# Kernel tuning notes

Hardware: AMD Instinct MI355X
Metric: run time of the kernel (lower is better)

## Reference

```python
import jax, jax.numpy as jnp
import numpy as np
from jax import lax

INPUT_SIZE = 256
HIDDEN = 256
NUM_CLASSES = 100
BLANK_ID = 3
B, T = 512, 128
STEPS = 26  # batch_max_length + 1


def setup_inputs() -> dict:
    key = jax.random.key(0)
    ks = jax.random.split(key, 16)
    s = lambda fan_in: 1.0 / np.sqrt(fan_in)
    inp = {
        "batch_H": jax.random.normal(ks[0], (B, T, INPUT_SIZE), dtype=jnp.float32),
        "text": jax.random.randint(ks[1], (B, STEPS), 0, NUM_CLASSES),
        "batch_max_length": 25,
        # AttentionCell params
        "W_i2h": jax.random.uniform(ks[2], (HIDDEN, INPUT_SIZE), minval=-s(INPUT_SIZE), maxval=s(INPUT_SIZE)),
        "W_h2h": jax.random.uniform(ks[3], (HIDDEN, HIDDEN), minval=-s(HIDDEN), maxval=s(HIDDEN)),
        "b_h2h": jax.random.uniform(ks[4], (HIDDEN,), minval=-s(HIDDEN), maxval=s(HIDDEN)),
        "W_score": jax.random.uniform(ks[5], (1, HIDDEN), minval=-s(HIDDEN), maxval=s(HIDDEN)),
        # LSTMCell params (PyTorch layout: gates order i, f, g, o)
        "W_ih": jax.random.uniform(ks[6], (4 * HIDDEN, INPUT_SIZE + NUM_CLASSES), minval=-s(HIDDEN), maxval=s(HIDDEN)),
        "W_hh": jax.random.uniform(ks[7], (4 * HIDDEN, HIDDEN), minval=-s(HIDDEN), maxval=s(HIDDEN)),
        "b_ih": jax.random.uniform(ks[8], (4 * HIDDEN,), minval=-s(HIDDEN), maxval=s(HIDDEN)),
        "b_hh": jax.random.uniform(ks[9], (4 * HIDDEN,), minval=-s(HIDDEN), maxval=s(HIDDEN)),
        # generator
        "W_gen": jax.random.uniform(ks[10], (NUM_CLASSES, HIDDEN), minval=-s(HIDDEN), maxval=s(HIDDEN)),
        "b_gen": jax.random.uniform(ks[11], (NUM_CLASSES,), minval=-s(HIDDEN), maxval=s(HIDDEN)),
    }
    return inp


def reference(batch_H, text, batch_max_length, W_i2h, W_h2h, b_h2h, W_score,
              W_ih, W_hh, b_ih, b_hh, W_gen, b_gen):
    Bsz = batch_H.shape[0]
    H = W_h2h.shape[0]
    num_classes = W_gen.shape[0]
    dt = batch_H.dtype

    # i2h(batch_H) is loop-invariant: hoist (same math as per-step recompute)
    proj_H = jnp.einsum("bti,hi->bth", batch_H, W_i2h)  # [B, T, H]

    def step(carry, tgt):
        h, c = carry
        proj_h = h @ W_h2h.T + b_h2h                      # [B, H]
        e = jnp.tanh(proj_H + proj_h[:, None, :]) @ W_score[0]  # [B, T]
        alpha = jax.nn.softmax(e, axis=1)
        context = jnp.einsum("bt,bti->bi", alpha, batch_H)  # [B, input]
        onehot = jax.nn.one_hot(tgt, num_classes, dtype=dt)
        x = jnp.concatenate([context, onehot], axis=1)
        gates = x @ W_ih.T + b_ih + h @ W_hh.T + b_hh      # [B, 4H]
        i, f, g, o = jnp.split(gates, 4, axis=1)
        c_new = jax.nn.sigmoid(f) * c + jax.nn.sigmoid(i) * jnp.tanh(g)
        h_new = jax.nn.sigmoid(o) * jnp.tanh(c_new)
        return (h_new, c_new), h_new

    h0 = jnp.zeros((Bsz, H), dtype=dt)
    c0 = jnp.zeros((Bsz, H), dtype=dt)
    _, hs = lax.scan(step, (h0, c0), text.T)   # hs: [steps, B, H]
    out_hid = jnp.transpose(hs, (1, 0, 2))      # [B, steps, H]
    logits = out_hid @ W_gen.T + b_gen          # [B, steps, num_classes]
    logits = logits.at[:, :, BLANK_ID].set(-10000.0)
    return logits
```

## Files before the change

kernel.cpp:

```cpp
#include <hip/hip_runtime.h>
#include <hip/hip_fp16.h>
#include <stdint.h>

typedef unsigned short u16;
typedef unsigned char u8;
typedef unsigned int u32;
typedef __attribute__((ext_vector_type(8))) short short8;
typedef __attribute__((ext_vector_type(4))) float f32x4;

#define NSTEP 26
#define NB 512
#define NT 128
#define NH 256
#define NCLS 100

#define SP 32.0f
#define SH 24.0f
#define SW 2000.0f
#define S8 127.0f

#if defined(__has_builtin)
#if __has_builtin(__builtin_amdgcn_sdot4)
#define HAS_SDOT4 1
#endif
#endif

__device__ __forceinline__ u16 f2bf(float f) {
    unsigned u = __float_as_uint(f);
    return (u16)((u + 0x7FFFu + ((u >> 16) & 1u)) >> 16);
}
__device__ __forceinline__ int q8i(float x, float s) {
    float v = fminf(fmaxf(x * s, -127.f), 127.f);
    return __float2int_rn(v);
}
__device__ __forceinline__ float fast_tanh(float x) {
    float e = __expf(2.f * x);
    return 1.f - 2.f / (e + 1.f);
}
__device__ __forceinline__ float fast_sig(float x) { return 1.f / (1.f + __expf(-x)); }
__device__ __forceinline__ void async_g2l(const void* g, void* l) {
    __builtin_amdgcn_global_load_lds((const __attribute__((address_space(1))) u32*)g,
                                     (__attribute__((address_space(3))) u32*)l, 16, 0, 0);
}

__global__ void prep_all(const float* __restrict__ W_h2h, const float* __restrict__ W_i2h,
                         const float* __restrict__ W_ih, const float* __restrict__ W_hh,
                         const float* __restrict__ b_ih, const float* __restrict__ b_hh,
                         const float* __restrict__ W_gen,
                         char* __restrict__ Wh2h_q8, u16* __restrict__ Wi2h_bf,
                         u16* __restrict__ Wcat3, float* __restrict__ bsum,
                         u16* __restrict__ WgenP, float* __restrict__ WohT) {
    int idx = blockIdx.x * 256 + threadIdx.x;
    if (idx < 65536) {
        Wh2h_q8[idx] = (char)q8i(W_h2h[idx], SW);
        Wi2h_bf[idx] = f2bf(W_i2h[idx]);
    }
    for (int i = idx; i < 16 * 16 * 4 * 64 * 8; i += 65536) {
        int j = i & 7, lane = (i >> 3) & 63, q = (i >> 9) & 3, ks = (i >> 11) & 15, ub = i >> 15;
        int lr = lane & 15, lq = lane >> 4;
        int rg = q * 256 + ub * 16 + lr;
        int k = ks * 32 + lq * 8 + j;
        float v = (k < 256) ? W_ih[(size_t)rg * 356 + k] : W_hh[(size_t)rg * 256 + (k - 256)];
        Wcat3[i] = f2bf(v);
    }
    for (int i = idx; i < 100 * 1024; i += 65536) {
        int t = i >> 10, rg = i & 1023;
        WohT[i] = W_ih[(size_t)rg * 356 + 256 + t];
    }
    if (idx < 1024) bsum[idx] = b_ih[idx] + b_hh[idx];
    if (idx < 32768) {
        int r = idx >> 8, ccol = idx & 255;
        WgenP[idx] = (r < NCLS) ? f2bf(W_gen[r * 256 + ccol]) : (u16)0;
    }
}

__launch_bounds__(512, 3)
__global__ void gemm_projH5(const float* __restrict__ bH, const u16* __restrict__ Wi2h_bf,
                            char* __restrict__ projF8, char* __restrict__ bHf8) {
    __shared__ char gsm[49152];
    u16* As[2] = {(u16*)gsm, (u16*)(gsm + 8192)};
    u16* Bs[2] = {(u16*)(gsm + 16384), (u16*)(gsm + 32768)};
    char* Tt = gsm;

    int b = blockIdx.x, tid = threadIdx.x;
    int wave = tid >> 6, lane = tid & 63, lr = lane & 15, lq = lane >> 4;
    int wm = wave >> 2, wn = wave & 3;
    int ar = tid >> 2, part = tid & 3;
    const float* asrc = bH + ((size_t)b * 128 + ar) * 256 + part * 8;
    f32x4 acc[4][4] = {};
    uint2 bh[8];

    auto stageB = [&](int kc, int buf) {
        for (int i = 0; i < 2; i++) {
            int ch = wave * 2 + i;
            int row = ch * 16 + (lane >> 2);
            const u16* g = Wi2h_bf + (size_t)row * 256 + kc * 32 + (lane & 3) * 8;
            async_g2l(g, (char*)Bs[buf] + ch * 1024 + lane * 16);
        }
    };
    auto writeA = [&](int kc, int buf, float4 v0, float4 v1) {
        u16* dst = As[buf] + ar * 32 + part * 8;
        dst[0] = f2bf(v0.x); dst[1] = f2bf(v0.y); dst[2] = f2bf(v0.z); dst[3] = f2bf(v0.w);
        dst[4] = f2bf(v1.x); dst[5] = f2bf(v1.y); dst[6] = f2bf(v1.z); dst[7] = f2bf(v1.w);
        uint p0 = (uint)(u8)q8i(v0.x, SH) | ((uint)(u8)q8i(v0.y, SH) << 8) |
                  ((uint)(u8)q8i(v0.z, SH) << 16) | ((uint)(u8)q8i(v0.w, SH) << 24);
        uint p1 = (uint)(u8)q8i(v1.x, SH) | ((uint)(u8)q8i(v1.y, SH) << 8) |
                  ((uint)(u8)q8i(v1.z, SH) << 16) | ((uint)(u8)q8i(v1.w, SH) << 24);
        bh[kc].x = p0; bh[kc].y = p1;
    };

    float4 a0 = *(const float4*)(asrc);
    float4 a1 = *(const float4*)(asrc + 4);
    stageB(0, 0);
    writeA(0, 0, a0, a1);
    __syncthreads();

    for (int kc = 0; kc < 8; kc++) {
        int cur = kc & 1, nxt = cur ^ 1;
        if (kc < 7) {
            stageB(kc + 1, nxt);
            a0 = *(const float4*)(asrc + (kc + 1) * 32);
            a1 = *(const float4*)(asrc + (kc + 1) * 32 + 4);
        }
        short8 af[4];
        for (int mi = 0; mi < 4; mi++)
            af[mi] = *(const short8*)(As[cur] + (wm * 64 + mi * 16 + lr) * 32 + lq * 8);
        for (int ni = 0; ni < 4; ni++) {
            short8 bf = *(const short8*)(Bs[cur] + (wn * 64 + ni * 16 + lr) * 32 + lq * 8);
            for (int mi = 0; mi < 4; mi++)
                acc[mi][ni] = __builtin_amdgcn_mfma_f32_16x16x32_bf16(af[mi], bf, acc[mi][ni], 0, 0, 0);
        }
        if (kc < 7) writeA(kc + 1, nxt, a0, a1);
        __syncthreads();
    }

    for (int kc = 0; kc < 8; kc++)
        *(uint2*)(bHf8 + (size_t)b * 32768 + ar * 256 + kc * 32 + part * 8) = bh[kc];

    for (int mi = 0; mi < 4; mi++)
        for (int ni = 0; ni < 4; ni++) {
            int h = wn * 64 + ni * 16 + lr;
            int t = wm * 64 + mi * 16 + lq * 4;
            f32x4 v = acc[mi][ni];
            uint pk = (uint)(u8)q8i(v[0], SP) | ((uint)(u8)q8i(v[1], SP) << 8) |
                      ((uint)(u8)q8i(v[2], SP) << 16) | ((uint)(u8)q8i(v[3], SP) << 24);
            *(uint*)(Tt + h * 144 + t) = pk;
        }
    __syncthreads();
    {
        int hrow = tid >> 1, half = tid & 1;
        const char* src = Tt + hrow * 144 + half * 64;
        char* dst = projF8 + (size_t)b * 32768 + hrow * 128 + half * 64;
        uint4 v0 = *(const uint4*)(src);
        uint4 v1 = *(const uint4*)(src + 16);
        uint4 v2 = *(const uint4*)(src + 32);
        uint4 v3 = *(const uint4*)(src + 48);
        *(uint4*)(dst) = v0; *(uint4*)(dst + 16) = v1;
        *(uint4*)(dst + 32) = v2; *(uint4*)(dst + 48) = v3;
    }
}

#define OFF_PROJ 0
#define OFF_BH   65536
#define OFF_XT   131072
#define OFF_ZB   133120
#define OFF_PH   133184
#define OFF_GC   135232
#define OFF_GH   143424
#define OFF_EP   151616
#define OFF_ES   155712
#define OFF_H8   156736
#define OFF_WS   157248
#define OFF_B2   158272
#define OFF_TG   159296
#define OFF_RI   159552
#define LDS_TOT  159616

__launch_bounds__(512, 1)
__global__ void step_loop7(const char* __restrict__ projF8, const char* __restrict__ bHf8,
                           const char* __restrict__ Wh2h_q8, const float* __restrict__ b_h2h,
                           const float* __restrict__ W_score, const u16* __restrict__ Wcat3,
                           const float* __restrict__ bsum, const float* __restrict__ WohT,
                           const int* __restrict__ text, u16* __restrict__ hbf_all) {
    __shared__ __align__(16) char Lm[LDS_TOT];
    u16* Xt = (u16*)(Lm + OFF_XT);
    u16* zb = (u16*)(Lm + OFF_ZB);
    float* phL = (float*)(Lm + OFF_PH);
    float* gcC = (float*)(Lm + OFF_GC);
    float* gcH = (float*)(Lm + OFF_GH);
    float* epL = (float*)(Lm + OFF_EP);
    float* esL = (float*)(Lm + OFF_ES);
    char* h8c = Lm + OFF_H8;
    float* wsL = (float*)(Lm + OFF_WS);
    float* b2L = (float*)(Lm + OFF_B2);
    int* tgL = (int*)(Lm + OFF_TG);
    float* riL = (float*)(Lm + OFF_RI);

    int blk = blockIdx.x, tid = threadIdx.x;
    int lane = tid & 63;
    int wv = tid >> 6;
    int lr = lane & 15, lq = lane >> 4;
    int rot = (blk >> 3) & 15;
    int rot7 = rot & 7;
    int tq = tid & 7, hg = (tid & 255) >> 3;
    int b = tid >> 8, htid = tid & 255;

    {
        const uint4* pg = (const uint4*)(projF8 + (size_t)blk * 65536);
        const uint4* bg = (const uint4*)(bHf8 + (size_t)blk * 65536);
#pragma unroll
        for (int q = 0; q < 8; q++) {
            int w = tid + q * 512;
            int c = w & 7;
            int R = (w >> 3) & 255;
            int b2 = w >> 11;
            uint4 v = pg[w];
            *(uint4*)(Lm + OFF_PROJ + b2 * 32768 + R * 128 + (((c ^ (R >> 3)) & 7) << 4)) = v;
            *(uint4*)(Lm + OFF_BH + w * 16) = bg[w];
        }
        if (tid < 128) *(uint*)(Lm + OFF_XT + 512 + tid * 4) = 0;
        else if (tid < 256) *(uint*)(Lm + OFF_XT + 1536 + (tid - 128) * 4) = 0;
        if (tid < 16) *(uint*)(Lm + OFF_ZB + tid * 4) = 0;
        if (tid < 256) { wsL[tid] = W_score[tid]; b2L[tid] = b_h2h[tid]; }
        if (tid < 52) {
            int bb = tid >= 26, st = tid - bb * 26;
            tgL[bb * 26 + st] = text[(blk * 2 + bb) * NSTEP + st];
        }
    }
    __syncthreads();

    float creg = 0.f;

    for (int s = 0; s < NSTEP; s++) {
        if (wv < 4) {
            {
                int u = tid;
                float v0, v1;
                if (s == 0) {
                    v0 = v1 = b2L[u];
                } else {
                    const uint4* wrow = (const uint4*)(Wh2h_q8 + (size_t)u * 256);
                    const uint4* hv0 = (const uint4*)(h8c);
                    const uint4* hv1 = (const uint4*)(h8c + 256);
                    int a0 = 0, a1 = 0;
#pragma unroll
                    for (int k = 0; k < 16; k++) {
                        uint4 w = wrow[k];
                        uint4 ha = hv0[k];
                        uint4 hb = hv1[k];
#ifdef HAS_SDOT4
                        a0 = __builtin_amdgcn_sdot4((int)w.x, (int)ha.x, a0, false);
                        a0 = __builtin_amdgcn_sdot4((int)w.y, (int)ha.y, a0, false);
                        a0 = __builtin_amdgcn_sdot4((int)w.z, (int)ha.z, a0, false);
                        a0 = __builtin_amdgcn_sdot4((int)w.w, (int)ha.w, a0, false);
                        a1 = __builtin_amdgcn_sdot4((int)w.x, (int)hb.x, a1, false);
                        a1 = __builtin_amdgcn_sdot4((int)w.y, (int)hb.y, a1, false);
                        a1 = __builtin_amdgcn_sdot4((int)w.z, (int)hb.z, a1, false);
                        a1 = __builtin_amdgcn_sdot4((int)w.w, (int)hb.w, a1, false);
#else
                        uint wv_[4] = {w.x, w.y, w.z, w.w};
                        uint ha_[4] = {ha.x, ha.y, ha.z, ha.w};
                        uint hb_[4] = {hb.x, hb.y, hb.z, hb.w};
                        for (int c = 0; c < 4; c++)
                            for (int by = 0; by < 32; by += 8) {
                                a0 += (int)(char)(wv_[c] >> by) * (int)(char)(ha_[c] >> by);
                                a1 += (int)(char)(wv_[c] >> by) * (int)(char)(hb_[c] >> by);
                            }
#endif
                    }
                    v0 = (float)a0 * (1.f / (SW * S8)) + b2L[u];
                    v1 = (float)a1 * (1.f / (SW * S8)) + b2L[u];
                }
                phL[u] = v0;
                phL[256 + u] = v1;
            }
            asm volatile("s_waitcnt lgkmcnt(0)" ::: "memory");
            {
                const __half2 c3 = __float2half2_rn(-0.0016249f), c2 = __float2half2_rn(0.031520f);
                const __half2 c1h = __float2half2_rn(-0.222110f), c0h = __float2half2_rn(0.962117f);
                const float inv = 1.f / SP;
                int t0e = tq * 16;
                int co = ((tq ^ hg) & 7) << 4;
                for (int bb = 0; bb < 2; bb++) {
                    __half2 acc2[8];
#pragma unroll
                    for (int q = 0; q < 8; q++) acc2[q] = __float2half2_rn(0.f);
                    const char* baseL = Lm + OFF_PROJ + bb * 32768 + co;
#pragma unroll
                    for (int hh = 0; hh < 8; hh++) {
                        int R = hg * 8 + hh;
                        uint4 uu = *(const uint4*)(baseL + R * 128);
                        float phv = phL[bb * 256 + R];
                        __half2 wv2 = __float2half2_rn(wsL[R]);
                        uint wq[4] = {uu.x, uu.y, uu.z, uu.w};
#pragma unroll
                        for (int wi = 0; wi < 4; wi++) {
                            uint w = wq[wi];
#pragma unroll
                            for (int pp = 0; pp < 2; pp++) {
                                float xa = fmaf((float)(char)(w >> (pp * 16)), inv, phv);
                                float xb = fmaf((float)(char)(w >> (pp * 16 + 8)), inv, phv);
                                xa = fminf(fmaxf(xa, -3.0f), 3.0f);
                                xb = fminf(fmaxf(xb, -3.0f), 3.0f);
                                __half2 x = __floats2half2_rn(xa, xb);
                                __half2 u2 = __hmul2(x, x);
                                __half2 p = __hfma2(__hfma2(__hfma2(c3, u2, c2), u2, c1h), u2, c0h);
                                acc2[wi * 2 + pp] = __hfma2(__hmul2(x, p), wv2, acc2[wi * 2 + pp]);
                            }
                        }
                    }
                    float a16[16];
#pragma unroll
                    for (int q = 0; q < 8; q++) {
                        a16[q * 2] = __low2float(acc2[q]);
                        a16[q * 2 + 1] = __high2float(acc2[q]);
                    }
#pragma unroll
                    for (int j = 0; j < 16; j++) {
                        float v = a16[j];
                        v += __shfl_xor(v, 8);
                        v += __shfl_xor(v, 16);
                        v += __shfl_xor(v, 32);
                        a16[j] = v;
                    }
                    if (lane < 8) {
                        int t0w = lane * 16;
#pragma unroll
                        for (int j = 0; j < 16; j++) epL[bb * 512 + (t0w + j) * 4 + wv] = a16[j];
                    }
                }
            }
        } else {
            int w4 = wv - 4;
            const u16* xsrc = (lr < 2) ? (Xt + lr * 512) : zb;
            int xstep = (lr < 2) ? 1 : 0;
#pragma unroll
            for (int r = 0; r < 4; r++) {
                int ub = (w4 * 4 + r + rot) & 15;
                f32x4 ac[4] = {};
                for (int kk = 0; kk < 8; kk++) {
                    int ks = 8 + ((kk + rot) & 7);
                    short8 af = *(const short8*)(xsrc + (ks * 32 + lq * 8) * xstep);
                    const u16* wb = Wcat3 + (size_t)((ub * 16 + ks) * 4) * 512 + lane * 8;
#pragma unroll
                    for (int g = 0; g < 4; g++)
                        ac[g] = __builtin_amdgcn_mfma_f32_16x16x32_bf16(
                            af, *(const short8*)(wb + g * 512), ac[g], 0, 0, 0);
                }
                if (lq == 0) {
#pragma unroll
                    for (int g = 0; g < 4; g++) {
                        gcH[(0 * 4 + g) * 256 + ub * 16 + lr] = ac[g][0];
                        gcH[(1 * 4 + g) * 256 + ub * 16 + lr] = ac[g][1];
                    }
                }
            }
        }
        __syncthreads();

        if (wv < 2) {
            int bb = wv;
            int t0 = lane * 2;
            float e0 = 0.f, e1 = 0.f;
#pragma unroll
            for (int w = 0; w < 4; w++) {
                e0 += epL[bb * 512 + t0 * 4 + w];
                e1 += epL[bb * 512 + (t0 + 1) * 4 + w];
            }
            float m = fmaxf(e0, e1);
            for (int o = 32; o >= 1; o >>= 1) m = fmaxf(m, __shfl_xor(m, o));
            float x0 = __expf(e0 - m), x1 = __expf(e1 - m);
            float ss = x0 + x1;
            for (int o = 32; o >= 1; o >>= 1) ss += __shfl_xor(ss, o);
            esL[bb * 128 + t0] = x0; esL[bb * 128 + t0 + 1] = x1;
            if (lane == 0) riL[bb] = 1.f / ss;
        }
        __syncthreads();

        {
            int slice = htid >> 6, ig = htid & 63;
            const char* bsrc = Lm + OFF_BH + b * 32768 + slice * 32 * 256 + ig * 4;
            const float* es = esL + b * 128 + slice * 32;
            float a0 = 0.f, a1 = 0.f, a2 = 0.f, a3 = 0.f;
#pragma unroll
            for (int t = 0; t < 32; t++) {
                float al = es[t];
                uint v = *(const uint*)(bsrc + t * 256);
                a0 += al * (float)(char)(v);
                a1 += al * (float)(char)(v >> 8);
                a2 += al * (float)(char)(v >> 16);
                a3 += al * (float)(char)(v >> 24);
            }
            float* cp = gcC + (b * 4 + slice) * 256 + ig * 4;
            cp[0] = a0; cp[1] = a1; cp[2] = a2; cp[3] = a3;
        }
        __syncthreads();

        {
            int i = htid;
            float sm = gcC[(b * 4 + 0) * 256 + i] + gcC[(b * 4 + 1) * 256 + i] +
                       gcC[(b * 4 + 2) * 256 + i] + gcC[(b * 4 + 3) * 256 + i];
            Xt[b * 512 + i] = f2bf(sm * riL[b] * (1.f / SH));
        }
        __syncthreads();

        {
            const u16* xsrc = (lr < 2) ? (Xt + lr * 512) : zb;
            int xstep = (lr < 2) ? 1 : 0;
            f32x4 ac0[4] = {}, ac1[4] = {};
            int ub0 = wv * 2, ub1 = wv * 2 + 1;
#pragma unroll 4
            for (int kk = 0; kk < 8; kk++) {
                int ks = (kk + rot7) & 7;
                short8 af = *(const short8*)(xsrc + (ks * 32 + lq * 8) * xstep);
                const u16* wb0 = Wcat3 + (size_t)((ub0 * 16 + ks) * 4) * 512 + lane * 8;
                const u16* wb1 = Wcat3 + (size_t)((ub1 * 16 + ks) * 4) * 512 + lane * 8;
#pragma unroll
                for (int g = 0; g < 4; g++) {
                    ac0[g] = __builtin_amdgcn_mfma_f32_16x16x32_bf16(
                        af, *(const short8*)(wb0 + g * 512), ac0[g], 0, 0, 0);
                    ac1[g] = __builtin_amdgcn_mfma_f32_16x16x32_bf16(
                        af, *(const short8*)(wb1 + g * 512), ac1[g], 0, 0, 0);
                }
            }
            if (lq == 0) {
#pragma unroll
                for (int g = 0; g < 4; g++) {
                    gcC[(0 * 4 + g) * 256 + ub0 * 16 + lr] = ac0[g][0];
                    gcC[(1 * 4 + g) * 256 + ub0 * 16 + lr] = ac0[g][1];
                    gcC[(0 * 4 + g) * 256 + ub1 * 16 + lr] = ac1[g][0];
                    gcC[(1 * 4 + g) * 256 + ub1 * 16 + lr] = ac1[g][1];
                }
            }
        }
        __syncthreads();

        {
            int u = htid;
            int tgt = tgL[b * 26 + s];
            const float* wt = WohT + (size_t)tgt * 1024;
            float gi = gcC[(b * 4 + 0) * 256 + u] + gcH[(b * 4 + 0) * 256 + u] + bsum[u] + wt[u];
            float gf = gcC[(b * 4 + 1) * 256 + u] + gcH[(b * 4 + 1) * 256 + u] + bsum[256 + u] + wt[256 + u];
            float gg = gcC[(b * 4 + 2) * 256 + u] + gcH[(b * 4 + 2) * 256 + u] + bsum[512 + u] + wt[512 + u];
            float go = gcC[(b * 4 + 3) * 256 + u] + gcH[(b * 4 + 3) * 256 + u] + bsum[768 + u] + wt[768 + u];
            float cn = fast_sig(gf) * creg + fast_sig(gi) * fast_tanh(gg);
            float hn = fast_sig(go) * fast_tanh(cn);
            creg = cn;
            hbf_all[(size_t)s * NB * NH + (size_t)(blk * 2 + b) * 256 + u] = f2bf(hn);
            h8c[b * 256 + u] = (char)q8i(hn, S8);
            Xt[b * 512 + 256 + u] = f2bf(hn);
        }
        __syncthreads();
    }
}

__launch_bounds__(256)
__global__ void gen_logits(const u16* __restrict__ hbf_all, const u16* __restrict__ WgenP,
                           const float* __restrict__ b_gen, float* __restrict__ out) {
    __shared__ u16 As[32 * 32];
    __shared__ u16 Bs[128 * 32];
    int mb = blockIdx.x;
    int tid = threadIdx.x;
    int wave = tid >> 6, lane = tid & 63, lr = lane & 15, lq = lane >> 4;
    int wm = wave >> 1, wn = wave & 1;
    f32x4 acc[4] = {};
    for (int kc = 0; kc < 256; kc += 32) {
        __syncthreads();
        {
            int r = tid >> 3, c4 = (tid & 7) * 4;
            *(ushort4*)(As + r * 32 + c4) =
                *(const ushort4*)(hbf_all + (size_t)(mb * 32 + r) * 256 + kc + c4);
        }
        {
            int r = tid >> 1, h16 = (tid & 1) * 16;
            const u16* src = WgenP + (size_t)r * 256 + kc + h16;
            u16* d = Bs + r * 32 + h16;
            *(ushort4*)(d) = *(const ushort4*)(src);
            *(ushort4*)(d + 4) = *(const ushort4*)(src + 4);
            *(ushort4*)(d + 8) = *(const ushort4*)(src + 8);
            *(ushort4*)(d + 12) = *(const ushort4*)(src + 12);
        }
        __syncthreads();
        short8 a = *reinterpret_cast<const short8*>(As + (wm * 16 + lr) * 32 + lq * 8);
        for (int ni = 0; ni < 4; ni++) {
            short8 bb = *reinterpret_cast<const short8*>(Bs + (wn * 64 + ni * 16 + lr) * 32 + lq * 8);
            acc[ni] = __builtin_amdgcn_mfma_f32_16x16x32_bf16(a, bb, acc[ni], 0, 0, 0);
        }
    }
    for (int ni = 0; ni < 4; ni++) {
        int cidx = wn * 64 + ni * 16 + lr;
        if (cidx >= NCLS) continue;
        float bg = b_gen[cidx];
        int mbase = mb * 32 + wm * 16 + lq * 4;
        for (int r = 0; r < 4; r++) {
            int mm = mbase + r;
            int s = mm >> 9;
            int bb_ = mm & 511;
            float v = (cidx == 3) ? -10000.f : (acc[ni][r] + bg);
            out[(size_t)bb_ * (NSTEP * NCLS) + s * NCLS + cidx] = v;
        }
    }
}

extern "C" void kernel_launch(void* const* d_in, const int* in_sizes, int n_in,
                              void* d_out, int out_size, void* d_ws, size_t ws_size,
                              hipStream_t stream) {
    const float* batch_H = (const float*)d_in[0];
    const int* text = (const int*)d_in[1];
    const float* W_i2h = (const float*)d_in[3];
    const float* W_h2h = (const float*)d_in[4];
    const float* b_h2h = (const float*)d_in[5];
    const float* W_score = (const float*)d_in[6];
    const float* W_ih = (const float*)d_in[7];
    const float* W_hh = (const float*)d_in[8];
    const float* b_ih = (const float*)d_in[9];
    const float* b_hh = (const float*)d_in[10];
    const float* W_gen = (const float*)d_in[11];
    const float* b_gen = (const float*)d_in[12];
    float* out = (float*)d_out;

    char* ws = (char*)d_ws;
    size_t off = 0;
    auto alloc = [&](size_t bytes) {
        void* p = ws + off;
        off += (bytes + 255) & ~(size_t)255;
        return p;
    };
    char* projF8 = (char*)alloc((size_t)16777216);
    char* bHf8 = (char*)alloc((size_t)16777216);
    char* Wh2h_q8 = (char*)alloc(65536);
    u16* Wi2h_bf = (u16*)alloc(65536 * 2);
    u16* Wcat3 = (u16*)alloc((size_t)524288 * 2);
    float* bsum = (float*)alloc(1024 * 4);
    u16* WgenP = (u16*)alloc(32768 * 2);
    float* WohT = (float*)alloc((size_t)102400 * 4);
    u16* hbf_all = (u16*)alloc((size_t)NSTEP * NB * NH * 2);

    prep_all<<<256, 256, 0, stream>>>(W_h2h, W_i2h, W_ih, W_hh, b_ih, b_hh, W_gen,
                                      Wh2h_q8, Wi2h_bf, Wcat3, bsum, WgenP, WohT);
    gemm_projH5<<<512, 512, 0, stream>>>(batch_H, Wi2h_bf, projF8, bHf8);
    step_loop7<<<256, 512, 0, stream>>>(projF8, bHf8, Wh2h_q8, b_h2h, W_score,
                                        Wcat3, bsum, WohT, text, hbf_all);
    gen_logits<<<416, 256, 0, stream>>>(hbf_all, WgenP, b_gen, out);
}
```

Baseline: 544.2 us.

## Quantize LSTM gate weights and inputs to int8 and use i8 MFMA

Switches the per-step LSTM gate GEMMs (context and hidden parts) from bf16 MFMA to int8 MFMA 16x16x64. Weights are prequantized to int8 in a repacked layout, the context and hidden vectors are stored as int8 in LDS, and the int32 accumulators are rescaled to float. This halves the weight bytes streamed from global/L2 each step and halves the number of MFMA issues. The cost is extra quantization error in the gate preactivations, which compounds over the recurrent steps.

```diff
diff --git a/kernel.cpp b/kernel.cpp
--- a/kernel.cpp
+++ b/kernel.cpp
@@ -7,6 +7,7 @@
 typedef unsigned int u32;
 typedef __attribute__((ext_vector_type(8))) short short8;
 typedef __attribute__((ext_vector_type(4))) float f32x4;
+typedef __attribute__((ext_vector_type(4))) int i32x4;
 
 #define NSTEP 26
 #define NB 512
@@ -48,20 +49,20 @@
                          const float* __restrict__ b_ih, const float* __restrict__ b_hh,
                          const float* __restrict__ W_gen,
                          char* __restrict__ Wh2h_q8, u16* __restrict__ Wi2h_bf,
-                         u16* __restrict__ Wcat3, float* __restrict__ bsum,
+                         char* __restrict__ Wcat8, float* __restrict__ bsum,
                          u16* __restrict__ WgenP, float* __restrict__ WohT) {
     int idx = blockIdx.x * 256 + threadIdx.x;
     if (idx < 65536) {
         Wh2h_q8[idx] = (char)q8i(W_h2h[idx], SW);
         Wi2h_bf[idx] = f2bf(W_i2h[idx]);
     }
-    for (int i = idx; i < 16 * 16 * 4 * 64 * 8; i += 65536) {
-        int j = i & 7, lane = (i >> 3) & 63, q = (i >> 9) & 3, ks = (i >> 11) & 15, ub = i >> 15;
+    for (int i = idx; i < 16 * 8 * 4 * 64 * 16; i += 65536) {
+        int j = i & 15, lane = (i >> 4) & 63, g = (i >> 10) & 3, ks64 = (i >> 12) & 7, ub = i >> 15;
         int lr = lane & 15, lq = lane >> 4;
-        int rg = q * 256 + ub * 16 + lr;
-        int k = ks * 32 + lq * 8 + j;
+        int rg = g * 256 + ub * 16 + lr;
+        int k = ks64 * 64 + lq * 16 + j;
         float v = (k < 256) ? W_ih[(size_t)rg * 356 + k] : W_hh[(size_t)rg * 256 + (k - 256)];
-        Wcat3[i] = f2bf(v);
+        Wcat8[i] = (char)q8i(v, SW);
     }
     for (int i = idx; i < 100 * 1024; i += 65536) {
         int t = i >> 10, rg = i & 1023;
@@ -162,29 +163,29 @@
 
 #define OFF_PROJ 0
 #define OFF_BH   65536
-#define OFF_XT   131072
-#define OFF_ZB   133120
-#define OFF_PH   133184
-#define OFF_GC   135232
-#define OFF_GH   143424
-#define OFF_EP   151616
-#define OFF_ES   155712
-#define OFF_H8   156736
-#define OFF_WS   157248
-#define OFF_B2   158272
-#define OFF_TG   159296
-#define OFF_RI   159552
-#define LDS_TOT  159616
+#define OFF_XQ   131072
+#define OFF_ZB   131584
+#define OFF_PH   131648
+#define OFF_GC   133696
+#define OFF_GH   141888
+#define OFF_EP   150080
+#define OFF_ES   154176
+#define OFF_H8   155200
+#define OFF_WS   155712
+#define OFF_B2   156736
+#define OFF_TG   157760
+#define OFF_RI   158016
+#define LDS_TOT  158080
 
 __launch_bounds__(512, 1)
-__global__ void step_loop7(const char* __restrict__ projF8, const char* __restrict__ bHf8,
+__global__ void step_loop8(const char* __restrict__ projF8, const char* __restrict__ bHf8,
                            const char* __restrict__ Wh2h_q8, const float* __restrict__ b_h2h,
-                           const float* __restrict__ W_score, const u16* __restrict__ Wcat3,
+                           const float* __restrict__ W_score, const char* __restrict__ Wcat8,
                            const float* __restrict__ bsum, const float* __restrict__ WohT,
                            const int* __restrict__ text, u16* __restrict__ hbf_all) {
     __shared__ __align__(16) char Lm[LDS_TOT];
-    u16* Xt = (u16*)(Lm + OFF_XT);
-    u16* zb = (u16*)(Lm + OFF_ZB);
+    char* Xq8 = Lm + OFF_XQ;
+    char* zbc = Lm + OFF_ZB;
     float* phL = (float*)(Lm + OFF_PH);
     float* gcC = (float*)(Lm + OFF_GC);
     float* gcH = (float*)(Lm + OFF_GH);
@@ -201,7 +202,6 @@
     int wv = tid >> 6;
     int lr = lane & 15, lq = lane >> 4;
     int rot = (blk >> 3) & 15;
-    int rot7 = rot & 7;
     int tq = tid & 7, hg = (tid & 255) >> 3;
     int b = tid >> 8, htid = tid & 255;
 
@@ -218,9 +218,8 @@
             *(uint4*)(Lm + OFF_PROJ + b2 * 32768 + R * 128 + (((c ^ (R >> 3)) & 7) << 4)) = v;
             *(uint4*)(Lm + OFF_BH + w * 16) = bg[w];
         }
-        if (tid < 128) *(uint*)(Lm + OFF_XT + 512 + tid * 4) = 0;
-        else if (tid < 256) *(uint*)(Lm + OFF_XT + 1536 + (tid - 128) * 4) = 0;
-        if (tid < 16) *(uint*)(Lm + OFF_ZB + tid * 4) = 0;
+        if (tid < 128) *(uint*)(h8c + tid * 4) = 0;
+        if (tid < 16) *(uint*)(zbc + tid * 4) = 0;
         if (tid < 256) { wsL[tid] = W_score[tid]; b2L[tid] = b_h2h[tid]; }
         if (tid < 52) {
             int bb = tid >= 26, st = tid - bb * 26;
@@ -332,26 +331,27 @@
             }
         } else {
             int w4 = wv - 4;
-            const u16* xsrc = (lr < 2) ? (Xt + lr * 512) : zb;
+            const char* xsH = (lr < 2) ? (h8c + lr * 256) : zbc;
             int xstep = (lr < 2) ? 1 : 0;
 #pragma unroll
             for (int r = 0; r < 4; r++) {
                 int ub = (w4 * 4 + r + rot) & 15;
-                f32x4 ac[4] = {};
-                for (int kk = 0; kk < 8; kk++) {
-                    int ks = 8 + ((kk + rot) & 7);
-                    short8 af = *(const short8*)(xsrc + (ks * 32 + lq * 8) * xstep);
-                    const u16* wb = Wcat3 + (size_t)((ub * 16 + ks) * 4) * 512 + lane * 8;
+                i32x4 ac[4] = {};
+#pragma unroll
+                for (int kk = 0; kk < 4; kk++) {
+                    int ks = (kk + rot) & 3;
+                    i32x4 av = *(const i32x4*)(xsH + (ks * 64 + lq * 16) * xstep);
+                    const char* wb = Wcat8 + (size_t)((ub * 8 + 4 + ks) * 4) * 1024 + lane * 16;
 #pragma unroll
                     for (int g = 0; g < 4; g++)
-                        ac[g] = __builtin_amdgcn_mfma_f32_16x16x32_bf16(
-                            af, *(const short8*)(wb + g * 512), ac[g], 0, 0, 0);
+                        ac[g] = __builtin_amdgcn_mfma_i32_16x16x64_i8(
+                            av, *(const i32x4*)(wb + g * 1024), ac[g], 0, 0, 0);
                 }
                 if (lq == 0) {
 #pragma unroll
                     for (int g = 0; g < 4; g++) {
-                        gcH[(0 * 4 + g) * 256 + ub * 16 + lr] = ac[g][0];
-                        gcH[(1 * 4 + g) * 256 + ub * 16 + lr] = ac[g][1];
+                        gcH[(0 * 4 + g) * 256 + ub * 16 + lr] = (float)ac[g][0] * (1.f / (SW * S8));
+                        gcH[(1 * 4 + g) * 256 + ub * 16 + lr] = (float)ac[g][1] * (1.f / (SW * S8));
                     }
                 }
             }
@@ -400,36 +400,36 @@
             int i = htid;
             float sm = gcC[(b * 4 + 0) * 256 + i] + gcC[(b * 4 + 1) * 256 + i] +
                        gcC[(b * 4 + 2) * 256 + i] + gcC[(b * 4 + 3) * 256 + i];
-            Xt[b * 512 + i] = f2bf(sm * riL[b] * (1.f / SH));
+            Xq8[b * 256 + i] = (char)q8i(sm * riL[b], 1.f);
         }
         __syncthreads();
 
         {
-            const u16* xsrc = (lr < 2) ? (Xt + lr * 512) : zb;
+            const char* xsC = (lr < 2) ? (Xq8 + lr * 256) : zbc;
             int xstep = (lr < 2) ? 1 : 0;
-            f32x4 ac0[4] = {}, ac1[4] = {};
+            i32x4 ac0[4] = {}, ac1[4] = {};
             int ub0 = wv * 2, ub1 = wv * 2 + 1;
-#pragma unroll 4
-            for (int kk = 0; kk < 8; kk++) {
-                int ks = (kk + rot7) & 7;
-                short8 af = *(const short8*)(xsrc + (ks * 32 + lq * 8) * xstep);
-                const u16* wb0 = Wcat3 + (size_t)((ub0 * 16 + ks) * 4) * 512 + lane * 8;
-                const u16* wb1 = Wcat3 + (size_t)((ub1 * 16 + ks) * 4) * 512 + lane * 8;
+#pragma unroll
+            for (int kk = 0; kk < 4; kk++) {
+                int ks = (kk + rot) & 3;
+                i32x4 av = *(const i32x4*)(xsC + (ks * 64 + lq * 16) * xstep);
+                const char* wb0 = Wcat8 + (size_t)((ub0 * 8 + ks) * 4) * 1024 + lane * 16;
+                const char* wb1 = Wcat8 + (size_t)((ub1 * 8 + ks) * 4) * 1024 + lane * 16;
 #pragma unroll
                 for (int g = 0; g < 4; g++) {
-                    ac0[g] = __builtin_amdgcn_mfma_f32_16x16x32_bf16(
-                        af, *(const short8*)(wb0 + g * 512), ac0[g], 0, 0, 0);
-                    ac1[g] = __builtin_amdgcn_mfma_f32_16x16x32_bf16(
-                        af, *(const short8*)(wb1 + g * 512), ac1[g], 0, 0, 0);
+                    ac0[g] = __builtin_amdgcn_mfma_i32_16x16x64_i8(
+                        av, *(const i32x4*)(wb0 + g * 1024), ac0[g], 0, 0, 0);
+                    ac1[g] = __builtin_amdgcn_mfma_i32_16x16x64_i8(
+                        av, *(const i32x4*)(wb1 + g * 1024), ac1[g], 0, 0, 0);
                 }
             }
             if (lq == 0) {
 #pragma unroll
                 for (int g = 0; g < 4; g++) {
-                    gcC[(0 * 4 + g) * 256 + ub0 * 16 + lr] = ac0[g][0];
-                    gcC[(1 * 4 + g) * 256 + ub0 * 16 + lr] = ac0[g][1];
-                    gcC[(0 * 4 + g) * 256 + ub1 * 16 + lr] = ac1[g][0];
-                    gcC[(1 * 4 + g) * 256 + ub1 * 16 + lr] = ac1[g][1];
+                    gcC[(0 * 4 + g) * 256 + ub0 * 16 + lr] = (float)ac0[g][0] * (1.f / (SW * SH));
+                    gcC[(1 * 4 + g) * 256 + ub0 * 16 + lr] = (float)ac0[g][1] * (1.f / (SW * SH));
+                    gcC[(0 * 4 + g) * 256 + ub1 * 16 + lr] = (float)ac1[g][0] * (1.f / (SW * SH));
+                    gcC[(1 * 4 + g) * 256 + ub1 * 16 + lr] = (float)ac1[g][1] * (1.f / (SW * SH));
                 }
             }
         }
@@ -448,7 +448,6 @@
             creg = cn;
             hbf_all[(size_t)s * NB * NH + (size_t)(blk * 2 + b) * 256 + u] = f2bf(hn);
             h8c[b * 256 + u] = (char)q8i(hn, S8);
-            Xt[b * 512 + 256 + u] = f2bf(hn);
         }
         __syncthreads();
     }
@@ -530,16 +529,16 @@
     char* bHf8 = (char*)alloc((size_t)16777216);
     char* Wh2h_q8 = (char*)alloc(65536);
     u16* Wi2h_bf = (u16*)alloc(65536 * 2);
-    u16* Wcat3 = (u16*)alloc((size_t)524288 * 2);
+    char* Wcat8 = (char*)alloc((size_t)524288);
     float* bsum = (float*)alloc(1024 * 4);
     u16* WgenP = (u16*)alloc(32768 * 2);
     float* WohT = (float*)alloc((size_t)102400 * 4);
     u16* hbf_all = (u16*)alloc((size_t)NSTEP * NB * NH * 2);
 
     prep_all<<<256, 256, 0, stream>>>(W_h2h, W_i2h, W_ih, W_hh, b_ih, b_hh, W_gen,
-                                      Wh2h_q8, Wi2h_bf, Wcat3, bsum, WgenP, WohT);
+                                      Wh2h_q8, Wi2h_bf, Wcat8, bsum, WgenP, WohT);
     gemm_projH5<<<512, 512, 0, stream>>>(batch_H, Wi2h_bf, projF8, bHf8);
-    step_loop7<<<256, 512, 0, stream>>>(projF8, bHf8, Wh2h_q8, b_h2h, W_score,
-                                        Wcat3, bsum, WohT, text, hbf_all);
+    step_loop8<<<256, 512, 0, stream>>>(projF8, bHf8, Wh2h_q8, b_h2h, W_score,
+                                        Wcat8, bsum, WohT, text, hbf_all);
     gen_logits<<<416, 256, 0, stream>>>(hbf_all, WgenP, b_gen, out);
 }
```

Measured after the change: 480.9 us. 1.13x faster.
